# Performance work log

Hardware: AMD Instinct MI355X
Metric: run time of the kernel (lower is better)

The kernel has to match this reference:

```python
import jax, jax.numpy as jnp
import numpy as np

N, E, D = 20000, 100000, 64   # nodes, edges, feature dim
H, C = 16, 64                  # heads, per-head channels
NEG_SLOPE = 0.2                # PyG GATConv default


def add_self_loops(edge_index, edge_attr, n):
    # PyG add_self_loops with fill_value='mean': self-loop edge_attr is the
    # mean of incoming edge_attr per destination node (0 if no in-edges).
    src, dst = edge_index[0], edge_index[1]
    cnt = jax.ops.segment_sum(jnp.ones((edge_attr.shape[0],), edge_attr.dtype), dst, num_segments=n)
    loop_ea = jax.ops.segment_sum(edge_attr, dst, num_segments=n) / jnp.maximum(cnt, 1.0)[:, None]
    ar = jnp.arange(n, dtype=src.dtype)
    return (jnp.concatenate([src, ar]), jnp.concatenate([dst, ar]),
            jnp.concatenate([edge_attr, loop_ea], axis=0))


def gat_conv(x, src, dst, ea, W, a_src, a_dst, We, a_e, b):
    n = x.shape[0]
    xp = (x @ W).reshape(n, H, C)                      # [N,H,C]
    al_s = jnp.einsum('nhc,hc->nh', xp, a_src)         # [N,H]
    al_d = jnp.einsum('nhc,hc->nh', xp, a_dst)         # [N,H]
    # fold lin_edge and att_edge: (ea @ We).view(E,H,C) . a_e == ea @ w_e
    w_e = (We.reshape(D, H, C) * a_e[None]).sum(-1)    # [D,H]
    al_e = ea @ w_e                                    # [E,H]
    alpha = jax.nn.leaky_relu(al_s[src] + al_d[dst] + al_e, NEG_SLOPE)
    # segment softmax over destination nodes
    m = jax.ops.segment_max(alpha, dst, num_segments=n)
    ex = jnp.exp(alpha - m[dst])
    den = jax.ops.segment_sum(ex, dst, num_segments=n)
    att = ex / (den[dst] + 1e-16)                      # [E,H]
    out = jax.ops.segment_sum(xp[src] * att[:, :, None], dst, num_segments=n)  # [N,H,C]
    return out.mean(axis=1) + b                        # concat=False -> head mean


def setup_inputs() -> dict:
    key = jax.random.key(0)
    ks = jax.random.split(key, 16)
    p = lambda k, shp: (0.1 * jax.random.normal(k, shp)).astype(jnp.float32)
    return {
        'x': jax.random.normal(ks[0], (N, D), dtype=jnp.float32),
        'edge_index': jax.random.randint(ks[1], (2, E), 0, N, dtype=jnp.int32),
        'edge_attr': jax.random.normal(ks[2], (E, D), dtype=jnp.float32),
        'W1': p(ks[3], (D, H * C)), 'att_src1': p(ks[4], (H, C)), 'att_dst1': p(ks[5], (H, C)),
        'We1': p(ks[6], (D, H * C)), 'att_e1': p(ks[7], (H, C)), 'b1': jnp.zeros((C,), jnp.float32),
        'W2': p(ks[8], (D, H * C)), 'att_src2': p(ks[9], (H, C)), 'att_dst2': p(ks[10], (H, C)),
        'We2': p(ks[11], (D, H * C)), 'att_e2': p(ks[12], (H, C)), 'b2': jnp.zeros((C,), jnp.float32),
    }


def reference(x, edge_index, edge_attr, W1, att_src1, att_dst1, We1, att_e1, b1,
              W2, att_src2, att_dst2, We2, att_e2, b2):
    n = x.shape[0]
    src, dst, ea = add_self_loops(edge_index, edge_attr, n)
    h = jax.nn.relu(gat_conv(x, src, dst, ea, W1, att_src1, att_dst1, We1, att_e1, b1))
    out = jax.nn.relu(gat_conv(h, src, dst, ea, W2, att_src2, att_dst2, We2, att_e2, b2))
    return out
```

## Files before the change

kernel.cpp:

```cpp
#include <hip/hip_runtime.h>

constexpr int TD  = 64;
constexpr int TH  = 16;
constexpr int TC  = 64;
constexpr int THC = TH * TC;

typedef short bf16x8 __attribute__((ext_vector_type(8)));
typedef unsigned short u16x8 __attribute__((ext_vector_type(8)));
typedef float f32x4 __attribute__((ext_vector_type(4)));

static __device__ __forceinline__ unsigned short f2bf(float f) {
  unsigned u = __float_as_uint(f);
  u += 0x7FFF + ((u >> 16) & 1);
  return (unsigned short)(u >> 16);
}
static __device__ __forceinline__ float bf2f(unsigned short h) {
  return __uint_as_float(((unsigned)h) << 16);
}


__global__ void k_count2(const int* __restrict__ src, const int* __restrict__ dst,
                         int E, int N, int* __restrict__ degd, int* __restrict__ degs) {
  int e = blockIdx.x * blockDim.x + threadIdx.x;
  if (e >= E + N) return;
  int s, d;
  if (e < E) { s = src[e]; d = dst[e]; } else { s = d = e - E; }
  atomicAdd(&degd[d], 1);
  atomicAdd(&degs[s], 1);
}

__global__ __launch_bounds__(1024) void k_scan2(
    const int* __restrict__ degd, int N,
    int* __restrict__ row_start, int* __restrict__ cursor,
    const int* __restrict__ degs,
    int* __restrict__ srow, int* __restrict__ scursor) {
  const int* dg = blockIdx.x ? degs : degd;
  int* rs = blockIdx.x ? srow : row_start;
  int* cu = blockIdx.x ? scursor : cursor;
  __shared__ int wsum[16];
  int t = threadIdx.x;
  int chunk = (N + 1023) / 1024;
  int lo = min(t * chunk, N), hi = min(lo + chunk, N);
  int s = 0;
  for (int i = lo; i < hi; ++i) s += dg[i];
  int lane = t & 63, wid = t >> 6;
  int v = s;
  for (int d = 1; d < 64; d <<= 1) {
    int u = __shfl_up(v, d, 64);
    if (lane >= d) v += u;
  }
  if (lane == 63) wsum[wid] = v;
  __syncthreads();
  if (t < 16) {
    int wv = wsum[t];
    for (int d = 1; d < 16; d <<= 1) {
      int u = __shfl_up(wv, d, 16);
      if (t >= d) wv += u;
    }
    wsum[t] = wv;
  }
  __syncthreads();
  int waveoff = wid ? wsum[wid - 1] : 0;
  int run = waveoff + (v - s);
  for (int i = lo; i < hi; ++i) {
    rs[i] = run; cu[i] = run; run += dg[i];
  }
  if (t == 1023) rs[N] = waveoff + v;
}

__global__ void k_scatter_dst(const int* __restrict__ src, const int* __restrict__ dst,
                              int E, int N, int* __restrict__ cursor,
                              int* __restrict__ eid, int* __restrict__ srcc,
                              int* __restrict__ inv) {
  int e = blockIdx.x * blockDim.x + threadIdx.x;
  if (e >= E + N) return;
  int s, d;
  if (e < E) { s = src[e]; d = dst[e]; } else { s = d = e - E; }
  int pos = atomicAdd(&cursor[d], 1);
  eid[pos] = e; srcc[pos] = s; inv[e] = pos;
}

__global__ void k_scatter_src(const int* __restrict__ src, int E, int N,
                              int* __restrict__ scursor, const int* __restrict__ inv,
                              int* __restrict__ smap) {
  int e = blockIdx.x * blockDim.x + threadIdx.x;
  if (e >= E + N) return;
  int s = (e < E) ? src[e] : (e - E);
  int j = atomicAdd(&scursor[s], 1);
  smap[j] = inv[e];
}


__global__ void k_prep_w(const float* __restrict__ W1, const float* __restrict__ W2,
                         unsigned short* __restrict__ Wbh, unsigned short* __restrict__ Wbl) {
  int t = blockIdx.x * 256 + threadIdx.x;
  if (t >= 2 * 64 * 2 * 64) return;
  int lane = t & 63, ks = (t >> 6) & 1, ct = (t >> 7) & 63, layer = t >> 13;
  const float* W = layer ? W2 : W1;
  int col = ct * 16 + (lane & 15);
  int kb = ks * 32 + ((lane >> 4) << 3);
  u16x8 H, L;
#pragma unroll
  for (int i = 0; i < 8; ++i) {
    float v = W[(size_t)(kb + i) * THC + col];
    unsigned short hi = f2bf(v);
    H[i] = hi;
    L[i] = f2bf(v - bf2f(hi));
  }
  *(u16x8*)&Wbh[(size_t)t * 8] = H;
  *(u16x8*)&Wbl[(size_t)t * 8] = L;
}

__global__ __launch_bounds__(256) void k_prep_x(const float* __restrict__ xin, int N, int Npad,
                                                unsigned short* __restrict__ xbh,
                                                unsigned short* __restrict__ xbl) {
  int t = blockIdx.x * 256 + threadIdx.x;
  if (t >= Npad * 8) return;
  int row = t >> 3, c8 = (t & 7) * 8;
  u16x8 H = {0, 0, 0, 0, 0, 0, 0, 0}, L = {0, 0, 0, 0, 0, 0, 0, 0};
  if (row < N) {
    float4 v0 = *(const float4*)&xin[(size_t)row * TD + c8];
    float4 v1 = *(const float4*)&xin[(size_t)row * TD + c8 + 4];
    float v[8] = {v0.x, v0.y, v0.z, v0.w, v1.x, v1.y, v1.z, v1.w};
#pragma unroll
    for (int i = 0; i < 8; ++i) {
      unsigned short hi = f2bf(v[i]);
      H[i] = hi;
      L[i] = f2bf(v[i] - bf2f(hi));
    }
  }
  *(u16x8*)&xbh[(size_t)row * TD + c8] = H;
  *(u16x8*)&xbl[(size_t)row * TD + c8] = L;
}


__global__ __launch_bounds__(256) void k_matmul_mfma(
    const unsigned short* __restrict__ xbh, const unsigned short* __restrict__ xbl,
    const unsigned short* __restrict__ Wbh, const unsigned short* __restrict__ Wbl,
    const float* __restrict__ a_src, const float* __restrict__ a_dst,
    int N, int nrb, float* __restrict__ xp,
    float* __restrict__ al_s, float* __restrict__ al_d) {
  int tid = threadIdx.x;
  int nwg = nrb * 8;
  int wg = blockIdx.x;
  int q = nwg >> 3, rm = nwg & 7;
  int xcd = wg & 7, off = wg >> 3;
  int g = (xcd < rm ? xcd * (q + 1) : rm * (q + 1) + (xcd - rm) * q) + off;
  int hp = g & 7;
  int rb = g >> 3;
  int r0 = rb * 64;
  int w = tid >> 6, l = tid & 63;

  int arow = r0 + w * 16 + (l & 15);
  const unsigned short* xh = xbh + (size_t)arow * TD + ((l >> 4) << 3);
  const unsigned short* xl = xbl + (size_t)arow * TD + ((l >> 4) << 3);
  bf16x8 ah0 = *(const bf16x8*)xh;
  bf16x8 ah1 = *(const bf16x8*)(xh + 32);
  bf16x8 alo0 = *(const bf16x8*)xl;
  bf16x8 alo1 = *(const bf16x8*)(xl + 32);

  f32x4 acc[8];
  int ct0 = hp * 8;
#pragma unroll
  for (int nt = 0; nt < 8; ++nt) {
    size_t base = ((size_t)(ct0 + nt) * 2) * 512 + l * 8;
    bf16x8 bh0 = *(const bf16x8*)&Wbh[base];
    bf16x8 bh1 = *(const bf16x8*)&Wbh[base + 512];
    bf16x8 bl0 = *(const bf16x8*)&Wbl[base];
    bf16x8 bl1 = *(const bf16x8*)&Wbl[base + 512];
    f32x4 a = {0.f, 0.f, 0.f, 0.f};
    a = __builtin_amdgcn_mfma_f32_16x16x32_bf16(ah0, bh0, a, 0, 0, 0);
    a = __builtin_amdgcn_mfma_f32_16x16x32_bf16(ah1, bh1, a, 0, 0, 0);
    a = __builtin_amdgcn_mfma_f32_16x16x32_bf16(ah0, bl0, a, 0, 0, 0);
    a = __builtin_amdgcn_mfma_f32_16x16x32_bf16(ah1, bl1, a, 0, 0, 0);
    a = __builtin_amdgcn_mfma_f32_16x16x32_bf16(alo0, bh0, a, 0, 0, 0);
    a = __builtin_amdgcn_mfma_f32_16x16x32_bf16(alo1, bh1, a, 0, 0, 0);
    acc[nt] = a;
  }

  int rbase = r0 + w * 16 + ((l >> 4) << 2);
  int cl = l & 15;
#pragma unroll
  for (int nt = 0; nt < 8; ++nt) {
    int colg = hp * 128 + nt * 16 + cl;
#pragma unroll
    for (int r = 0; r < 4; ++r) {
      int rowg = rbase + r;
      if (rowg < N) xp[(size_t)rowg * THC + colg] = acc[nt][r];
    }
  }
#pragma unroll
  for (int hh = 0; hh < 2; ++hh) {
    int h = 2 * hp + hh;
    float as0 = a_src[h * TC + 0 * 16 + cl], as1 = a_src[h * TC + 1 * 16 + cl];
    float as2 = a_src[h * TC + 2 * 16 + cl], as3 = a_src[h * TC + 3 * 16 + cl];
    float ad0 = a_dst[h * TC + 0 * 16 + cl], ad1 = a_dst[h * TC + 1 * 16 + cl];
    float ad2 = a_dst[h * TC + 2 * 16 + cl], ad3 = a_dst[h * TC + 3 * 16 + cl];
#pragma unroll
    for (int r = 0; r < 4; ++r) {
      float ps = acc[hh * 4 + 0][r] * as0 + acc[hh * 4 + 1][r] * as1 +
                 acc[hh * 4 + 2][r] * as2 + acc[hh * 4 + 3][r] * as3;
      float pd = acc[hh * 4 + 0][r] * ad0 + acc[hh * 4 + 1][r] * ad1 +
                 acc[hh * 4 + 2][r] * ad2 + acc[hh * 4 + 3][r] * ad3;
      for (int m = 8; m >= 1; m >>= 1) {
        ps += __shfl_xor(ps, m, 16);
        pd += __shfl_xor(pd, m, 16);
      }
      int rowg = rbase + r;
      if (cl == 0 && rowg < N) { al_s[rowg * TH + h] = ps; al_d[rowg * TH + h] = pd; }
    }
  }
}


__global__ void k_we2(const float* __restrict__ We1, const float* __restrict__ ae1,
                      const float* __restrict__ We2, const float* __restrict__ ae2,
                      float* __restrict__ w_e) {
  int t = blockIdx.x * blockDim.x + threadIdx.x;
  if (t >= 2 * TD * TH) return;
  int layer = t >> 10, tt = t & 1023;
  int d = tt >> 4, h = tt & 15;
  const float* We = layer ? We2 : We1;
  const float* ae = layer ? ae2 : ae1;
  float s = 0.f;
  for (int c = 0; c < TC; ++c) s += We[(size_t)d * THC + h * TC + c] * ae[h * TC + c];
  w_e[t] = s;
}

__global__ void k_pack_we(const float* __restrict__ w_e,
                          unsigned short* __restrict__ Webh,
                          unsigned short* __restrict__ Webl) {
  int t = threadIdx.x;
  int lane = t & 63, ks = (t >> 6) & 1, layer = t >> 7;
  int h = lane & 15;
  int kb = ks * 32 + ((lane >> 4) << 3);
  u16x8 H, L;
#pragma unroll
  for (int i = 0; i < 8; ++i) {
    float v = w_e[layer * (TD * TH) + (kb + i) * TH + h];
    unsigned short hi = f2bf(v);
    H[i] = hi;
    L[i] = f2bf(v - bf2f(hi));
  }
  *(u16x8*)&Webh[(size_t)t * 8] = H;
  *(u16x8*)&Webl[(size_t)t * 8] = L;
}

__global__ __launch_bounds__(256) void k_al_e_mfma(
    const float* __restrict__ ea,
    const unsigned short* __restrict__ Webh, const unsigned short* __restrict__ Webl,
    int E, float* __restrict__ ale1, float* __restrict__ ale2) {
  int tid = threadIdx.x;
  int w = tid >> 6, l = tid & 63;
  int e0 = blockIdx.x * 64 + w * 16;
  int arow = e0 + (l & 15);
  int koff = (l >> 4) << 3;
  float a0[8], a1[8];
  if (arow < E) {
    float4 v0 = *(const float4*)&ea[(size_t)arow * TD + koff];
    float4 v1 = *(const float4*)&ea[(size_t)arow * TD + koff + 4];
    float4 v2 = *(const float4*)&ea[(size_t)arow * TD + 32 + koff];
    float4 v3 = *(const float4*)&ea[(size_t)arow * TD + 32 + koff + 4];
    a0[0] = v0.x; a0[1] = v0.y; a0[2] = v0.z; a0[3] = v0.w;
    a0[4] = v1.x; a0[5] = v1.y; a0[6] = v1.z; a0[7] = v1.w;
    a1[0] = v2.x; a1[1] = v2.y; a1[2] = v2.z; a1[3] = v2.w;
    a1[4] = v3.x; a1[5] = v3.y; a1[6] = v3.z; a1[7] = v3.w;
  } else {
#pragma unroll
    for (int i = 0; i < 8; ++i) { a0[i] = 0.f; a1[i] = 0.f; }
  }
  bf16x8 ah0, alo0, ah1, alo1;
#pragma unroll
  for (int i = 0; i < 8; ++i) {
    unsigned short h0 = f2bf(a0[i]);
    ah0[i] = (short)h0; alo0[i] = (short)f2bf(a0[i] - bf2f(h0));
    unsigned short h1 = f2bf(a1[i]);
    ah1[i] = (short)h1; alo1[i] = (short)f2bf(a1[i] - bf2f(h1));
  }

  f32x4 acc0 = {0.f, 0.f, 0.f, 0.f}, acc1 = {0.f, 0.f, 0.f, 0.f};
#pragma unroll
  for (int ks = 0; ks < 2; ++ks) {
    bf16x8 ah = ks ? ah1 : ah0;
    bf16x8 alo = ks ? alo1 : alo0;
    size_t b0 = (size_t)ks * 512 + l * 8;
    size_t b1 = (size_t)(2 + ks) * 512 + l * 8;
    bf16x8 bh_0 = *(const bf16x8*)&Webh[b0];
    bf16x8 bl_0 = *(const bf16x8*)&Webl[b0];
    bf16x8 bh_1 = *(const bf16x8*)&Webh[b1];
    bf16x8 bl_1 = *(const bf16x8*)&Webl[b1];
    acc0 = __builtin_amdgcn_mfma_f32_16x16x32_bf16(ah, bh_0, acc0, 0, 0, 0);
    acc0 = __builtin_amdgcn_mfma_f32_16x16x32_bf16(ah, bl_0, acc0, 0, 0, 0);
    acc0 = __builtin_amdgcn_mfma_f32_16x16x32_bf16(alo, bh_0, acc0, 0, 0, 0);
    acc1 = __builtin_amdgcn_mfma_f32_16x16x32_bf16(ah, bh_1, acc1, 0, 0, 0);
    acc1 = __builtin_amdgcn_mfma_f32_16x16x32_bf16(ah, bl_1, acc1, 0, 0, 0);
    acc1 = __builtin_amdgcn_mfma_f32_16x16x32_bf16(alo, bh_1, acc1, 0, 0, 0);
  }

  int rbase = e0 + ((l >> 4) << 2);
  int h = l & 15;
#pragma unroll
  for (int r = 0; r < 4; ++r) {
    int e = rbase + r;
    if (e < E) {
      ale1[(size_t)e * TH + h] = acc0[r];
      ale2[(size_t)e * TH + h] = acc1[r];
    }
  }
}


__global__ __launch_bounds__(256) void k_att(
    const float* __restrict__ al_s, const float* __restrict__ al_d,
    const float* __restrict__ ale, const int* __restrict__ row_start,
    const int* __restrict__ eid, const int* __restrict__ srcc,
    int E, int N, float* __restrict__ att) {
  int tid = threadIdx.x;
  int n = blockIdx.x * 4 + (tid >> 6);
  if (n >= N) return;
  int lane = tid & 63;
  int h = lane & 15, slot = lane >> 4;
  int beg = row_start[n], end = row_start[n + 1], deg = end - beg;
  float ald = al_d[n * TH + h];

  float a0 = 0.f, a1 = 0.f, a2 = 0.f, a3 = 0.f;
  float asum = 0.f;
  int selfp = -1;
  int cnt = 0;
  for (int p = slot; p < deg; p += 4, ++cnt) {
    int i = beg + p;
    int e = eid[i], s = srcc[i];
    float av = 0.f;
    if (e < E) { av = ale[(size_t)e * TH + h]; asum += av; }
    else selfp = p;
    float a = al_s[s * TH + h] + ald + av;
    if (cnt == 0) a0 = a; else if (cnt == 1) a1 = a;
    else if (cnt == 2) a2 = a; else if (cnt == 3) a3 = a;
  }
  asum += __shfl_xor(asum, 16);
  asum += __shfl_xor(asum, 32);
  float lale = asum / (float)max(deg - 1, 1);

  auto fin = [&](float a, int p) -> float {
    if (p == selfp) a += lale;
    return (a > 0.f) ? a : 0.2f * a;
  };
  auto raw = [&](int p) -> float {
    int i = beg + p;
    int e = eid[i], s = srcc[i];
    float av = (e < E) ? ale[(size_t)e * TH + h] : 0.f;
    return al_s[s * TH + h] + ald + av;
  };

  float mloc = -1e30f;
  cnt = 0;
  for (int p = slot; p < deg; p += 4, ++cnt) {
    float a;
    if      (cnt == 0) { a0 = fin(a0, p); a = a0; }
    else if (cnt == 1) { a1 = fin(a1, p); a = a1; }
    else if (cnt == 2) { a2 = fin(a2, p); a = a2; }
    else if (cnt == 3) { a3 = fin(a3, p); a = a3; }
    else a = fin(raw(p), p);
    mloc = fmaxf(mloc, a);
  }
  mloc = fmaxf(mloc, __shfl_xor(mloc, 16));
  mloc = fmaxf(mloc, __shfl_xor(mloc, 32));

  float dloc = 0.f;
  cnt = 0;
  for (int p = slot; p < deg; p += 4, ++cnt) {
    float a = (cnt == 0) ? a0 : (cnt == 1) ? a1 : (cnt == 2) ? a2 : (cnt == 3) ? a3
              : fin(raw(p), p);
    dloc += expf(a - mloc);
  }
  dloc += __shfl_xor(dloc, 16);
  dloc += __shfl_xor(dloc, 32);
  float dinv = 1.f / (dloc + 1e-16f);

  cnt = 0;
  for (int p = slot; p < deg; p += 4, ++cnt) {
    float a = (cnt == 0) ? a0 : (cnt == 1) ? a1 : (cnt == 2) ? a2 : (cnt == 3) ? a3
              : fin(raw(p), p);
    att[(size_t)(beg + p) * TH + h] = expf(a - mloc) * dinv;
  }
}

__global__ __launch_bounds__(256) void k_csc_z(const float* __restrict__ xp,
                                               const float* __restrict__ att,
                                               const int* __restrict__ srow,
                                               const int* __restrict__ smap,
                                               int N, float* __restrict__ z) {
  int tid = threadIdx.x;
  int s = blockIdx.x * 4 + (tid >> 6);
  if (s >= N) return;
  int lane = tid & 63;
  int slot = lane >> 4, c4 = (lane & 15) * 4;
  float4 xf[16];
#pragma unroll
  for (int h = 0; h < TH; ++h)
    xf[h] = *(const float4*)&xp[(size_t)s * THC + h * 64 + c4];
  int beg = srow[s], end = srow[s + 1];
  for (int j = beg + slot; j < end; j += 4) {
    int i = smap[j];
    const float* ar = &att[(size_t)i * TH];
    float4 a0 = *(const float4*)&ar[0];
    float4 a1 = *(const float4*)&ar[4];
    float4 a2 = *(const float4*)&ar[8];
    float4 a3 = *(const float4*)&ar[12];
    float aw[16] = {a0.x, a0.y, a0.z, a0.w, a1.x, a1.y, a1.z, a1.w,
                    a2.x, a2.y, a2.z, a2.w, a3.x, a3.y, a3.z, a3.w};
    float4 acc = make_float4(0.f, 0.f, 0.f, 0.f);
#pragma unroll
    for (int hh = 0; hh < TH; ++hh) {
      acc.x += aw[hh] * xf[hh].x; acc.y += aw[hh] * xf[hh].y;
      acc.z += aw[hh] * xf[hh].z; acc.w += aw[hh] * xf[hh].w;
    }
    *(float4*)&z[(size_t)i * 64 + c4] = acc;
  }
}

__global__ __launch_bounds__(256) void k_sum_z(const float* __restrict__ z,
                                               const int* __restrict__ row_start,
                                               const float* __restrict__ bias, int N,
                                               float* __restrict__ out,
                                               unsigned short* __restrict__ obh,
                                               unsigned short* __restrict__ obl) {
  int tid = threadIdx.x;
  int n = blockIdx.x * 16 + (tid >> 4);
  int c4 = (tid & 15) * 4;
  if (n >= N) return;
  int beg = row_start[n], end = row_start[n + 1];
  float4 acc = make_float4(0.f, 0.f, 0.f, 0.f);
  for (int i = beg; i < end; ++i) {
    float4 v = *(const float4*)&z[(size_t)i * 64 + c4];
    acc.x += v.x; acc.y += v.y; acc.z += v.z; acc.w += v.w;
  }
  float4 b = *(const float4*)&bias[c4];
  float o[4];
  o[0] = fmaxf(acc.x * (1.0f / TH) + b.x, 0.f);
  o[1] = fmaxf(acc.y * (1.0f / TH) + b.y, 0.f);
  o[2] = fmaxf(acc.z * (1.0f / TH) + b.z, 0.f);
  o[3] = fmaxf(acc.w * (1.0f / TH) + b.w, 0.f);
  if (out) *(float4*)&out[(size_t)n * 64 + c4] = make_float4(o[0], o[1], o[2], o[3]);
  if (obh) {
    unsigned H32[2], L32[2];
#pragma unroll
    for (int p = 0; p < 2; ++p) {
      unsigned short h0 = f2bf(o[2 * p]), h1 = f2bf(o[2 * p + 1]);
      unsigned short l0 = f2bf(o[2 * p] - bf2f(h0)), l1 = f2bf(o[2 * p + 1] - bf2f(h1));
      H32[p] = (unsigned)h0 | ((unsigned)h1 << 16);
      L32[p] = (unsigned)l0 | ((unsigned)l1 << 16);
    }
    *(uint2*)&obh[(size_t)n * TD + c4] = make_uint2(H32[0], H32[1]);
    *(uint2*)&obl[(size_t)n * TD + c4] = make_uint2(L32[0], L32[1]);
  }
}


extern "C" void kernel_launch(void* const* d_in, const int* in_sizes, int n_in,
                              void* d_out, int out_size, void* d_ws, size_t ws_size,
                              hipStream_t stream) {
  const float* x   = (const float*)d_in[0];
  const int*   ei  = (const int*)d_in[1];
  const float* ea  = (const float*)d_in[2];
  const float* W1  = (const float*)d_in[3];
  const float* as1 = (const float*)d_in[4];
  const float* ad1 = (const float*)d_in[5];
  const float* We1 = (const float*)d_in[6];
  const float* ae1 = (const float*)d_in[7];
  const float* b1  = (const float*)d_in[8];
  const float* W2  = (const float*)d_in[9];
  const float* as2 = (const float*)d_in[10];
  const float* ad2 = (const float*)d_in[11];
  const float* We2 = (const float*)d_in[12];
  const float* ae2 = (const float*)d_in[13];
  const float* b2  = (const float*)d_in[14];

  const int N  = in_sizes[0] / TD;
  const int E  = in_sizes[1] / 2;
  const int EN = E + N;
  const int* srcA = ei;
  const int* dstA = ei + E;

  char* w = (char*)d_ws;
  auto alloc = [&](size_t bytes) {
    char* p = w;
    w += (bytes + 255) & ~(size_t)255;
    return p;
  };
  int*   deg2      = (int*)alloc((size_t)2 * N * 4);
  int*   degd      = deg2;
  int*   degs      = deg2 + N;
  int*   row_start = (int*)alloc((size_t)(N + 1) * 4);
  int*   srow      = (int*)alloc((size_t)(N + 1) * 4);
  int*   cursor    = (int*)alloc((size_t)N * 4);
  int*   scursor   = (int*)alloc((size_t)N * 4);
  int*   eid       = (int*)alloc((size_t)EN * 4);
  int*   srcc      = (int*)alloc((size_t)EN * 4);
  int*   inv       = (int*)alloc((size_t)EN * 4);
  int*   smap      = (int*)alloc((size_t)EN * 4);
  float* xp        = (float*)alloc((size_t)N * THC * 4);
  float* al_s      = (float*)alloc((size_t)N * TH * 4);
  float* al_d      = (float*)alloc((size_t)N * TH * 4);
  float* ale1      = (float*)alloc((size_t)E * TH * 4);
  float* ale2      = (float*)alloc((size_t)E * TH * 4);
  float* att       = (float*)alloc((size_t)EN * TH * 4);
  float* z         = (float*)alloc((size_t)EN * TC * 4);
  float* w_e       = (float*)alloc((size_t)2 * TD * TH * 4);
  const int nrb  = (N + 63) / 64;
  const int Npad = nrb * 64;
  unsigned short* xbh = (unsigned short*)alloc((size_t)Npad * TD * 2);
  unsigned short* xbl = (unsigned short*)alloc((size_t)Npad * TD * 2);
  unsigned short* Wbh = (unsigned short*)alloc((size_t)2 * 64 * 2 * 64 * 8 * 2);
  unsigned short* Wbl = (unsigned short*)alloc((size_t)2 * 64 * 2 * 64 * 8 * 2);
  unsigned short* Webh = (unsigned short*)alloc((size_t)4 * 512 * 2);
  unsigned short* Webl = (unsigned short*)alloc((size_t)4 * 512 * 2);

  hipMemsetAsync(deg2, 0, (size_t)2 * N * 4, stream);
  k_count2<<<(EN + 255) / 256, 256, 0, stream>>>(srcA, dstA, E, N, degd, degs);
  k_scan2<<<2, 1024, 0, stream>>>(degd, N, row_start, cursor, degs, srow, scursor);
  k_scatter_dst<<<(EN + 255) / 256, 256, 0, stream>>>(srcA, dstA, E, N, cursor, eid, srcc, inv);
  k_scatter_src<<<(EN + 255) / 256, 256, 0, stream>>>(srcA, E, N, scursor, inv, smap);

  k_prep_w<<<(2 * 64 * 2 * 64 + 255) / 256, 256, 0, stream>>>(W1, W2, Wbh, Wbl);
  k_we2<<<8, 256, 0, stream>>>(We1, ae1, We2, ae2, w_e);
  k_pack_we<<<1, 256, 0, stream>>>(w_e, Webh, Webl);
  k_al_e_mfma<<<(E + 63) / 64, 256, 0, stream>>>(ea, Webh, Webl, E, ale1, ale2);

  const int mmgrid = nrb * 8;
  const size_t WBL = 64 * 2 * 64 * 8;

  k_prep_x<<<(Npad * 8 + 255) / 256, 256, 0, stream>>>(x, N, Npad, xbh, xbl);
  k_matmul_mfma<<<mmgrid, 256, 0, stream>>>(xbh, xbl, Wbh, Wbl, as1, ad1,
                                            N, nrb, xp, al_s, al_d);
  k_att<<<(N + 3) / 4, 256, 0, stream>>>(al_s, al_d, ale1, row_start, eid, srcc, E, N, att);
  k_csc_z<<<(N + 3) / 4, 256, 0, stream>>>(xp, att, srow, smap, N, z);
  k_sum_z<<<(N + 15) / 16, 256, 0, stream>>>(z, row_start, b1, N, nullptr, xbh, xbl);

  k_matmul_mfma<<<mmgrid, 256, 0, stream>>>(xbh, xbl, Wbh + WBL, Wbl + WBL, as2, ad2,
                                            N, nrb, xp, al_s, al_d);
  k_att<<<(N + 3) / 4, 256, 0, stream>>>(al_s, al_d, ale2, row_start, eid, srcc, E, N, att);
  k_csc_z<<<(N + 3) / 4, 256, 0, stream>>>(xp, att, srow, smap, N, z);
  k_sum_z<<<(N + 15) / 16, 256, 0, stream>>>(z, row_start, b2, N, (float*)d_out, nullptr, nullptr);
}
```

Baseline: 240.1 us.

## Fuse scatter kernels, fold bf16 split into matmul, merge w_e pack, simplify csc_z

Merges the two CSR/CSC scatter kernels into one, which drops the inv array. Fuses the We·att_e reduction with its bf16 hi/lo packing into a single kernel. Moves the x→bf16 hi/lo split into the matmul's A-load so that k_prep_x and the bf16 outputs of k_sum_z go away, and layer 1 output now goes to an fp32 buffer that reuses ale1. Also changes k_csc_z from float4-per-lane over 4 edge slots to one channel per lane walking edges serially, which may reduce parallelism per source node; reusing ale1 as hbuf is safe only because ale1 is consumed before it is overwritten.

```diff
diff --git a/kernel.cpp b/kernel.cpp
--- a/kernel.cpp
+++ b/kernel.cpp
@@ -68,26 +68,18 @@
   if (t == 1023) rs[N] = waveoff + v;
 }
 
-__global__ void k_scatter_dst(const int* __restrict__ src, const int* __restrict__ dst,
-                              int E, int N, int* __restrict__ cursor,
-                              int* __restrict__ eid, int* __restrict__ srcc,
-                              int* __restrict__ inv) {
+__global__ void k_scatter(const int* __restrict__ src, const int* __restrict__ dst,
+                          int E, int N, int* __restrict__ cursor, int* __restrict__ scursor,
+                          int* __restrict__ eid, int* __restrict__ srcc,
+                          int* __restrict__ smap) {
   int e = blockIdx.x * blockDim.x + threadIdx.x;
   if (e >= E + N) return;
   int s, d;
   if (e < E) { s = src[e]; d = dst[e]; } else { s = d = e - E; }
   int pos = atomicAdd(&cursor[d], 1);
-  eid[pos] = e; srcc[pos] = s; inv[e] = pos;
-}
-
-__global__ void k_scatter_src(const int* __restrict__ src, int E, int N,
-                              int* __restrict__ scursor, const int* __restrict__ inv,
-                              int* __restrict__ smap) {
-  int e = blockIdx.x * blockDim.x + threadIdx.x;
-  if (e >= E + N) return;
-  int s = (e < E) ? src[e] : (e - E);
+  eid[pos] = e; srcc[pos] = s;
   int j = atomicAdd(&scursor[s], 1);
-  smap[j] = inv[e];
+  smap[j] = pos;
 }
 
 
@@ -111,31 +103,33 @@
   *(u16x8*)&Wbl[(size_t)t * 8] = L;
 }
 
-__global__ __launch_bounds__(256) void k_prep_x(const float* __restrict__ xin, int N, int Npad,
-                                                unsigned short* __restrict__ xbh,
-                                                unsigned short* __restrict__ xbl) {
-  int t = blockIdx.x * 256 + threadIdx.x;
-  if (t >= Npad * 8) return;
-  int row = t >> 3, c8 = (t & 7) * 8;
-  u16x8 H = {0, 0, 0, 0, 0, 0, 0, 0}, L = {0, 0, 0, 0, 0, 0, 0, 0};
-  if (row < N) {
-    float4 v0 = *(const float4*)&xin[(size_t)row * TD + c8];
-    float4 v1 = *(const float4*)&xin[(size_t)row * TD + c8 + 4];
-    float v[8] = {v0.x, v0.y, v0.z, v0.w, v1.x, v1.y, v1.z, v1.w};
-#pragma unroll
-    for (int i = 0; i < 8; ++i) {
-      unsigned short hi = f2bf(v[i]);
-      H[i] = hi;
-      L[i] = f2bf(v[i] - bf2f(hi));
-    }
-  }
-  *(u16x8*)&xbh[(size_t)row * TD + c8] = H;
-  *(u16x8*)&xbl[(size_t)row * TD + c8] = L;
+__global__ void k_we_pack(const float* __restrict__ We1, const float* __restrict__ ae1,
+                          const float* __restrict__ We2, const float* __restrict__ ae2,
+                          unsigned short* __restrict__ Webh,
+                          unsigned short* __restrict__ Webl) {
+  int t = threadIdx.x;
+  int lane = t & 63, ks = (t >> 6) & 1, layer = t >> 7;
+  const float* We = layer ? We2 : We1;
+  const float* ae = layer ? ae2 : ae1;
+  int h = lane & 15;
+  int kb = ks * 32 + ((lane >> 4) << 3);
+  u16x8 H, L;
+#pragma unroll
+  for (int i = 0; i < 8; ++i) {
+    int d = kb + i;
+    float s = 0.f;
+    for (int c = 0; c < TC; ++c) s += We[(size_t)d * THC + h * TC + c] * ae[h * TC + c];
+    unsigned short hi = f2bf(s);
+    H[i] = hi;
+    L[i] = f2bf(s - bf2f(hi));
+  }
+  *(u16x8*)&Webh[(size_t)t * 8] = H;
+  *(u16x8*)&Webl[(size_t)t * 8] = L;
 }
 
 
 __global__ __launch_bounds__(256) void k_matmul_mfma(
-    const unsigned short* __restrict__ xbh, const unsigned short* __restrict__ xbl,
+    const float* __restrict__ xin,
     const unsigned short* __restrict__ Wbh, const unsigned short* __restrict__ Wbl,
     const float* __restrict__ a_src, const float* __restrict__ a_dst,
     int N, int nrb, float* __restrict__ xp,
@@ -152,12 +146,29 @@
   int w = tid >> 6, l = tid & 63;
 
   int arow = r0 + w * 16 + (l & 15);
-  const unsigned short* xh = xbh + (size_t)arow * TD + ((l >> 4) << 3);
-  const unsigned short* xl = xbl + (size_t)arow * TD + ((l >> 4) << 3);
-  bf16x8 ah0 = *(const bf16x8*)xh;
-  bf16x8 ah1 = *(const bf16x8*)(xh + 32);
-  bf16x8 alo0 = *(const bf16x8*)xl;
-  bf16x8 alo1 = *(const bf16x8*)(xl + 32);
+  int koff = (l >> 4) << 3;
+  float a0[8], a1[8];
+  if (arow < N) {
+    float4 v0 = *(const float4*)&xin[(size_t)arow * TD + koff];
+    float4 v1 = *(const float4*)&xin[(size_t)arow * TD + koff + 4];
+    float4 v2 = *(const float4*)&xin[(size_t)arow * TD + 32 + koff];
+    float4 v3 = *(const float4*)&xin[(size_t)arow * TD + 32 + koff + 4];
+    a0[0] = v0.x; a0[1] = v0.y; a0[2] = v0.z; a0[3] = v0.w;
+    a0[4] = v1.x; a0[5] = v1.y; a0[6] = v1.z; a0[7] = v1.w;
+    a1[0] = v2.x; a1[1] = v2.y; a1[2] = v2.z; a1[3] = v2.w;
+    a1[4] = v3.x; a1[5] = v3.y; a1[6] = v3.z; a1[7] = v3.w;
+  } else {
+#pragma unroll
+    for (int i = 0; i < 8; ++i) { a0[i] = 0.f; a1[i] = 0.f; }
+  }
+  bf16x8 ah0, alo0, ah1, alo1;
+#pragma unroll
+  for (int i = 0; i < 8; ++i) {
+    unsigned short h0 = f2bf(a0[i]);
+    ah0[i] = (short)h0; alo0[i] = (short)f2bf(a0[i] - bf2f(h0));
+    unsigned short h1 = f2bf(a1[i]);
+    ah1[i] = (short)h1; alo1[i] = (short)f2bf(a1[i] - bf2f(h1));
+  }
 
   f32x4 acc[8];
   int ct0 = hp * 8;
@@ -212,39 +223,6 @@
   }
 }
 
-
-__global__ void k_we2(const float* __restrict__ We1, const float* __restrict__ ae1,
-                      const float* __restrict__ We2, const float* __restrict__ ae2,
-                      float* __restrict__ w_e) {
-  int t = blockIdx.x * blockDim.x + threadIdx.x;
-  if (t >= 2 * TD * TH) return;
-  int layer = t >> 10, tt = t & 1023;
-  int d = tt >> 4, h = tt & 15;
-  const float* We = layer ? We2 : We1;
-  const float* ae = layer ? ae2 : ae1;
-  float s = 0.f;
-  for (int c = 0; c < TC; ++c) s += We[(size_t)d * THC + h * TC + c] * ae[h * TC + c];
-  w_e[t] = s;
-}
-
-__global__ void k_pack_we(const float* __restrict__ w_e,
-                          unsigned short* __restrict__ Webh,
-                          unsigned short* __restrict__ Webl) {
-  int t = threadIdx.x;
-  int lane = t & 63, ks = (t >> 6) & 1, layer = t >> 7;
-  int h = lane & 15;
-  int kb = ks * 32 + ((lane >> 4) << 3);
-  u16x8 H, L;
-#pragma unroll
-  for (int i = 0; i < 8; ++i) {
-    float v = w_e[layer * (TD * TH) + (kb + i) * TH + h];
-    unsigned short hi = f2bf(v);
-    H[i] = hi;
-    L[i] = f2bf(v - bf2f(hi));
-  }
-  *(u16x8*)&Webh[(size_t)t * 8] = H;
-  *(u16x8*)&Webl[(size_t)t * 8] = L;
-}
 
 __global__ __launch_bounds__(256) void k_al_e_mfma(
     const float* __restrict__ ea,
@@ -393,14 +371,13 @@
   int tid = threadIdx.x;
   int s = blockIdx.x * 4 + (tid >> 6);
   if (s >= N) return;
-  int lane = tid & 63;
-  int slot = lane >> 4, c4 = (lane & 15) * 4;
-  float4 xf[16];
+  int c = tid & 63;
+  float xf[16];
 #pragma unroll
   for (int h = 0; h < TH; ++h)
-    xf[h] = *(const float4*)&xp[(size_t)s * THC + h * 64 + c4];
+    xf[h] = xp[(size_t)s * THC + h * 64 + c];
   int beg = srow[s], end = srow[s + 1];
-  for (int j = beg + slot; j < end; j += 4) {
+  for (int j = beg; j < end; ++j) {
     int i = smap[j];
     const float* ar = &att[(size_t)i * TH];
     float4 a0 = *(const float4*)&ar[0];
@@ -409,22 +386,17 @@
     float4 a3 = *(const float4*)&ar[12];
     float aw[16] = {a0.x, a0.y, a0.z, a0.w, a1.x, a1.y, a1.z, a1.w,
                     a2.x, a2.y, a2.z, a2.w, a3.x, a3.y, a3.z, a3.w};
-    float4 acc = make_float4(0.f, 0.f, 0.f, 0.f);
-#pragma unroll
-    for (int hh = 0; hh < TH; ++hh) {
-      acc.x += aw[hh] * xf[hh].x; acc.y += aw[hh] * xf[hh].y;
-      acc.z += aw[hh] * xf[hh].z; acc.w += aw[hh] * xf[hh].w;
-    }
-    *(float4*)&z[(size_t)i * 64 + c4] = acc;
+    float acc = 0.f;
+#pragma unroll
+    for (int hh = 0; hh < TH; ++hh) acc += aw[hh] * xf[hh];
+    z[(size_t)i * 64 + c] = acc;
   }
 }
 
 __global__ __launch_bounds__(256) void k_sum_z(const float* __restrict__ z,
                                                const int* __restrict__ row_start,
                                                const float* __restrict__ bias, int N,
-                                               float* __restrict__ out,
-                                               unsigned short* __restrict__ obh,
-                                               unsigned short* __restrict__ obl) {
+                                               float* __restrict__ out) {
   int tid = threadIdx.x;
   int n = blockIdx.x * 16 + (tid >> 4);
   int c4 = (tid & 15) * 4;
@@ -436,24 +408,12 @@
     acc.x += v.x; acc.y += v.y; acc.z += v.z; acc.w += v.w;
   }
   float4 b = *(const float4*)&bias[c4];
-  float o[4];
-  o[0] = fmaxf(acc.x * (1.0f / TH) + b.x, 0.f);
-  o[1] = fmaxf(acc.y * (1.0f / TH) + b.y, 0.f);
-  o[2] = fmaxf(acc.z * (1.0f / TH) + b.z, 0.f);
-  o[3] = fmaxf(acc.w * (1.0f / TH) + b.w, 0.f);
-  if (out) *(float4*)&out[(size_t)n * 64 + c4] = make_float4(o[0], o[1], o[2], o[3]);
-  if (obh) {
-    unsigned H32[2], L32[2];
-#pragma unroll
-    for (int p = 0; p < 2; ++p) {
-      unsigned short h0 = f2bf(o[2 * p]), h1 = f2bf(o[2 * p + 1]);
-      unsigned short l0 = f2bf(o[2 * p] - bf2f(h0)), l1 = f2bf(o[2 * p + 1] - bf2f(h1));
-      H32[p] = (unsigned)h0 | ((unsigned)h1 << 16);
-      L32[p] = (unsigned)l0 | ((unsigned)l1 << 16);
-    }
-    *(uint2*)&obh[(size_t)n * TD + c4] = make_uint2(H32[0], H32[1]);
-    *(uint2*)&obl[(size_t)n * TD + c4] = make_uint2(L32[0], L32[1]);
-  }
+  float4 o;
+  o.x = fmaxf(acc.x * (1.0f / TH) + b.x, 0.f);
+  o.y = fmaxf(acc.y * (1.0f / TH) + b.y, 0.f);
+  o.z = fmaxf(acc.z * (1.0f / TH) + b.z, 0.f);
+  o.w = fmaxf(acc.w * (1.0f / TH) + b.w, 0.f);
+  *(float4*)&out[(size_t)n * 64 + c4] = o;
 }
 
 
@@ -497,7 +457,6 @@
   int*   scursor   = (int*)alloc((size_t)N * 4);
   int*   eid       = (int*)alloc((size_t)EN * 4);
   int*   srcc      = (int*)alloc((size_t)EN * 4);
-  int*   inv       = (int*)alloc((size_t)EN * 4);
   int*   smap      = (int*)alloc((size_t)EN * 4);
   float* xp        = (float*)alloc((size_t)N * THC * 4);
   float* al_s      = (float*)alloc((size_t)N * TH * 4);
@@ -506,40 +465,35 @@
   float* ale2      = (float*)alloc((size_t)E * TH * 4);
   float* att       = (float*)alloc((size_t)EN * TH * 4);
   float* z         = (float*)alloc((size_t)EN * TC * 4);
-  float* w_e       = (float*)alloc((size_t)2 * TD * TH * 4);
-  const int nrb  = (N + 63) / 64;
-  const int Npad = nrb * 64;
-  unsigned short* xbh = (unsigned short*)alloc((size_t)Npad * TD * 2);
-  unsigned short* xbl = (unsigned short*)alloc((size_t)Npad * TD * 2);
   unsigned short* Wbh = (unsigned short*)alloc((size_t)2 * 64 * 2 * 64 * 8 * 2);
   unsigned short* Wbl = (unsigned short*)alloc((size_t)2 * 64 * 2 * 64 * 8 * 2);
   unsigned short* Webh = (unsigned short*)alloc((size_t)4 * 512 * 2);
   unsigned short* Webl = (unsigned short*)alloc((size_t)4 * 512 * 2);
+  float* hbuf      = (float*)ale1;
 
   hipMemsetAsync(deg2, 0, (size_t)2 * N * 4, stream);
   k_count2<<<(EN + 255) / 256, 256, 0, stream>>>(srcA, dstA, E, N, degd, degs);
   k_scan2<<<2, 1024, 0, stream>>>(degd, N, row_start, cursor, degs, srow, scursor);
-  k_scatter_dst<<<(EN + 255) / 256, 256, 0, stream>>>(srcA, dstA, E, N, cursor, eid, srcc, inv);
-  k_scatter_src<<<(EN + 255) / 256, 256, 0, stream>>>(srcA, E, N, scursor, inv, smap);
+  k_scatter<<<(EN + 255) / 256, 256, 0, stream>>>(srcA, dstA, E, N, cursor, scursor,
+                                                  eid, srcc, smap);
 
   k_prep_w<<<(2 * 64 * 2 * 64 + 255) / 256, 256, 0, stream>>>(W1, W2, Wbh, Wbl);
-  k_we2<<<8, 256, 0, stream>>>(We1, ae1, We2, ae2, w_e);
-  k_pack_we<<<1, 256, 0, stream>>>(w_e, Webh, Webl);
+  k_we_pack<<<1, 256, 0, stream>>>(We1, ae1, We2, ae2, Webh, Webl);
   k_al_e_mfma<<<(E + 63) / 64, 256, 0, stream>>>(ea, Webh, Webl, E, ale1, ale2);
 
+  const int nrb = (N + 63) / 64;
   const int mmgrid = nrb * 8;
   const size_t WBL = 64 * 2 * 64 * 8;
 
-  k_prep_x<<<(Npad * 8 + 255) / 256, 256, 0, stream>>>(x, N, Npad, xbh, xbl);
-  k_matmul_mfma<<<mmgrid, 256, 0, stream>>>(xbh, xbl, Wbh, Wbl, as1, ad1,
+  k_matmul_mfma<<<mmgrid, 256, 0, stream>>>(x, Wbh, Wbl, as1, ad1,
                                             N, nrb, xp, al_s, al_d);
   k_att<<<(N + 3) / 4, 256, 0, stream>>>(al_s, al_d, ale1, row_start, eid, srcc, E, N, att);
   k_csc_z<<<(N + 3) / 4, 256, 0, stream>>>(xp, att, srow, smap, N, z);
-  k_sum_z<<<(N + 15) / 16, 256, 0, stream>>>(z, row_start, b1, N, nullptr, xbh, xbl);
-
-  k_matmul_mfma<<<mmgrid, 256, 0, stream>>>(xbh, xbl, Wbh + WBL, Wbl + WBL, as2, ad2,
+  k_sum_z<<<(N + 15) / 16, 256, 0, stream>>>(z, row_start, b1, N, hbuf);
+
+  k_matmul_mfma<<<mmgrid, 256, 0, stream>>>(hbuf, Wbh + WBL, Wbl + WBL, as2, ad2,
                                             N, nrb, xp, al_s, al_d);
   k_att<<<(N + 3) / 4, 256, 0, stream>>>(al_s, al_d, ale2, row_start, eid, srcc, E, N, att);
   k_csc_z<<<(N + 3) / 4, 256, 0, stream>>>(xp, att, srow, smap, N, z);
-  k_sum_z<<<(N + 15) / 16, 256, 0, stream>>>(z, row_start, b2, N, (float*)d_out, nullptr, nullptr);
-}
+  k_sum_z<<<(N + 15) / 16, 256, 0, stream>>>(z, row_start, b2, N, (float*)d_out);
+}
```

Result: slower. 276.2 us (+15.0%).
